# Optimization experiments

Hardware: AMD Instinct MI355X
Metric: run time of the kernel (lower is better)

## Reference

```python
import jax, jax.numpy as jnp
import numpy as np

N_NODES = 100000


def gcn_conv(x, src, dst, deg_inv_sqrt, W, b, n):
    # GCNConv: h = D^{-1/2} (A + I) D^{-1/2} (x W) + b
    h = x @ W                                   # [N, out]
    norm = deg_inv_sqrt[src] * deg_inv_sqrt[dst]  # [E+N]
    msg = h[src] * norm[:, None]                # gather + scale
    out = jax.ops.segment_sum(msg, dst, num_segments=n)  # scatter-add
    return out + b


def setup_inputs() -> dict:
    key = jax.random.key(0)
    k1, k2, k3, k4 = jax.random.split(key, 4)
    N, E, IN, H, C = N_NODES, 1600000, 256, 128, 16
    x = jax.random.normal(k1, (N, IN), dtype=jnp.float32)
    edge_index = jax.random.randint(k2, (2, E), 0, N, dtype=jnp.int64)
    W1 = jax.random.normal(k3, (IN, H), dtype=jnp.float32) * (1.0 / np.sqrt(IN))
    b1 = jnp.zeros((H,), dtype=jnp.float32)
    W2 = jax.random.normal(k4, (H, C), dtype=jnp.float32) * (1.0 / np.sqrt(H))
    b2 = jnp.zeros((C,), dtype=jnp.float32)
    return {"x": x, "edge_index": edge_index, "W1": W1, "b1": b1, "W2": W2, "b2": b2}


def reference(x, edge_index, W1, b1, W2, b2):
    n = x.shape[0]
    loop = jnp.arange(n, dtype=edge_index.dtype)
    src = jnp.concatenate([edge_index[0], loop])  # add self-loops
    dst = jnp.concatenate([edge_index[1], loop])
    deg = jax.ops.segment_sum(jnp.ones_like(src, dtype=x.dtype), dst, num_segments=n)
    deg_inv_sqrt = jax.lax.rsqrt(deg)  # deg >= 1 due to self-loops

    h = gcn_conv(x, src, dst, deg_inv_sqrt, W1, b1, n)
    h = jax.nn.relu(h)
    # dropout is identity in eval mode
    out = gcn_conv(h, src, dst, deg_inv_sqrt, W2, b2, n)
    return jax.nn.log_softmax(out, axis=1)
```

## Files before the change

kernel.cpp:

```cpp
#include <hip/hip_runtime.h>
#include <math.h>

#define IN_DIM 256
#define H_DIM  128
#define C_DIM  16
#define BK_SHIFT 8
#define BK_CAP   6144
#define CHUNK    4096

typedef __attribute__((ext_vector_type(8))) short bf16x8;
typedef __attribute__((ext_vector_type(4))) float f32x4;

__device__ __forceinline__ ushort f2bf(float f) {
    uint u = __float_as_uint(f);
    u += 0x7fffu + ((u >> 16) & 1u);
    return (ushort)(u >> 16);
}
__device__ __forceinline__ float bflo(uint v) { return __uint_as_float(v << 16); }
__device__ __forceinline__ float bfhi(uint v) { return __uint_as_float(v & 0xffff0000u); }
__device__ __forceinline__ uint pk2(float a, float b) {
    return (uint)f2bf(a) | ((uint)f2bf(b) << 16);
}

__global__ void k_zero(int* __restrict__ p, int n) {
    int i = blockIdx.x * blockDim.x + threadIdx.x;
    if (i < n) p[i] = 0;
}

__global__ __launch_bounds__(256) void k_part(const int* __restrict__ esrc, const int* __restrict__ edst, int E,
                                              int* __restrict__ bcnt, int2* __restrict__ part) {
    __shared__ int sh_cnt[512];
    __shared__ int sh_base[512];
    __shared__ int sh_gbase[512];
    __shared__ int sh_scan[256];
    __shared__ int2 sh_rec[CHUNK];
    int t = threadIdx.x;
    int c0 = blockIdx.x * CHUNK;
    int cnt = min(CHUNK, E - c0);
    sh_cnt[t] = 0; sh_cnt[t + 256] = 0;
    __syncthreads();
    int srcv[16], dstv[16], lrank[16];
#pragma unroll
    for (int j = 0; j < 16; j++) {
        int li = j * 256 + t;
        if (li < cnt) {
            srcv[j] = esrc[c0 + li]; dstv[j] = edst[c0 + li];
            lrank[j] = atomicAdd(&sh_cnt[dstv[j] >> BK_SHIFT], 1);
        }
    }
    __syncthreads();
    int pairsum = sh_cnt[2 * t] + sh_cnt[2 * t + 1];
    sh_scan[t] = pairsum;
    __syncthreads();
    for (int off = 1; off < 256; off <<= 1) {
        int x = 0;
        if (t >= off) x = sh_scan[t - off];
        __syncthreads();
        if (t >= off) sh_scan[t] += x;
        __syncthreads();
    }
    int excl = sh_scan[t] - pairsum;
    sh_base[2 * t] = excl;
    sh_base[2 * t + 1] = excl + sh_cnt[2 * t];
    __syncthreads();
    for (int b = t; b < 512; b += 256) {
        int c = sh_cnt[b];
        if (c > 0) sh_gbase[b] = atomicAdd(&bcnt[b], c);
    }
#pragma unroll
    for (int j = 0; j < 16; j++) {
        int li = j * 256 + t;
        if (li < cnt) {
            int b = dstv[j] >> BK_SHIFT;
            sh_rec[sh_base[b] + lrank[j]] = make_int2(srcv[j], dstv[j]);
        }
    }
    __syncthreads();
    for (int idx = t; idx < cnt; idx += 256) {
        int2 r = sh_rec[idx];
        int b = r.y >> BK_SHIFT;
        int pos = sh_gbase[b] + (idx - sh_base[b]);
        if (pos < BK_CAP) part[(size_t)b * BK_CAP + pos] = r;
    }
}

__global__ __launch_bounds__(256) void k_bscan(const int* __restrict__ bcnt, int* __restrict__ bkbase,
                                               int* __restrict__ offsets, int N) {
    __shared__ int sh_scan[256];
    int t = threadIdx.x;
    int a0 = bcnt[2 * t], a1 = bcnt[2 * t + 1];
    int pairsum = a0 + a1;
    sh_scan[t] = pairsum;
    __syncthreads();
    for (int off = 1; off < 256; off <<= 1) {
        int x = 0;
        if (t >= off) x = sh_scan[t - off];
        __syncthreads();
        if (t >= off) sh_scan[t] += x;
        __syncthreads();
    }
    int excl = sh_scan[t] - pairsum;
    bkbase[2 * t] = excl;
    bkbase[2 * t + 1] = excl + a0;
    if (t == 255) offsets[N] = sh_scan[255];
}

__global__ __launch_bounds__(256) void k_bsort(const int* __restrict__ bcnt, const int* __restrict__ bkbase,
                                               const int2* __restrict__ part,
                                               float* __restrict__ dis, int* __restrict__ offsets,
                                               int* __restrict__ csr, int N) {
    __shared__ int hist[256];
    __shared__ int run[256];
    __shared__ int srt[BK_CAP];
    int b = blockIdx.x, t = threadIdx.x;
    hist[t] = 0;
    __syncthreads();
    int cnt = min(bcnt[b], BK_CAP);
    const int2* bp = &part[(size_t)b * BK_CAP];
    for (int idx = t; idx < cnt; idx += 256)
        atomicAdd(&hist[bp[idx].y & 255], 1);
    __syncthreads();
    int v = hist[t];
    run[t] = v;
    __syncthreads();
    for (int off = 1; off < 256; off <<= 1) {
        int x = 0;
        if (t >= off) x = run[t - off];
        __syncthreads();
        if (t >= off) run[t] += x;
        __syncthreads();
    }
    int start = run[t] - v;
    int base = bkbase[b];
    int node = b * 256 + t;
    if (node < N) {
        dis[node] = rsqrtf((float)(v + 1));
        offsets[node] = base + start;
    }
    __syncthreads();
    run[t] = start;
    __syncthreads();
    for (int idx = t; idx < cnt; idx += 256) {
        int2 r = bp[idx];
        int lpos = atomicAdd(&run[r.y & 255], 1);
        srt[lpos] = r.x;
    }
    __syncthreads();
    for (int idx = t; idx < cnt; idx += 256)
        csr[base + idx] = srt[idx];
}

__global__ void k_w1cast(const float* __restrict__ W1, ushort* __restrict__ W1T) {
    int n = blockIdx.x, k = threadIdx.x;
    W1T[n * 256 + k] = f2bf(W1[k * 128 + n]);
}

__global__ __launch_bounds__(256) void k_gemm1(const float* __restrict__ x,
                                               const ushort* __restrict__ W1T,
                                               ushort* __restrict__ h1, int N) {
    __shared__ ushort Al[128 * 64];
    __shared__ ushort Bl[128 * 64];
    int tid = threadIdx.x;
    int lane = tid & 63, wid = tid >> 6;
    int wr = wid >> 1, wc = wid & 1;
    int r0 = blockIdx.x * 128;
    int row16 = lane & 15, kgrp = lane >> 4;

    f32x4 acc[4][4];
#pragma unroll
    for (int i = 0; i < 4; i++)
#pragma unroll
        for (int j = 0; j < 4; j++) acc[i][j] = (f32x4){0.f, 0.f, 0.f, 0.f};

    int srow = tid >> 1, shalf = tid & 1;

    for (int k0 = 0; k0 < 256; k0 += 64) {
        {
            int gr = r0 + srow;
            float4 f[8];
            if (gr < N) {
                const float* xp = &x[(size_t)gr * 256 + k0 + shalf * 32];
#pragma unroll
                for (int j = 0; j < 8; j++) f[j] = *(const float4*)&xp[j * 4];
            } else {
#pragma unroll
                for (int j = 0; j < 8; j++) f[j] = make_float4(0.f, 0.f, 0.f, 0.f);
            }
#pragma unroll
            for (int j = 0; j < 4; j++) {
                uint4 w;
                w.x = pk2(f[2 * j].x, f[2 * j].y);
                w.y = pk2(f[2 * j].z, f[2 * j].w);
                w.z = pk2(f[2 * j + 1].x, f[2 * j + 1].y);
                w.w = pk2(f[2 * j + 1].z, f[2 * j + 1].w);
                int idx = (srow * 64 + shalf * 32 + j * 8) ^ ((srow & 7) << 3);
                *(uint4*)&Al[idx] = w;
            }
        }
        {
            const ushort* wp = &W1T[srow * 256 + k0 + shalf * 32];
#pragma unroll
            for (int j = 0; j < 4; j++) {
                uint4 w = *(const uint4*)&wp[j * 8];
                int idx = (srow * 64 + shalf * 32 + j * 8) ^ ((srow & 7) << 3);
                *(uint4*)&Bl[idx] = w;
            }
        }
        __syncthreads();
#pragma unroll
        for (int kk = 0; kk < 2; kk++) {
            bf16x8 a[4], b[4];
#pragma unroll
            for (int mi = 0; mi < 4; mi++) {
                int r = wr * 64 + mi * 16 + row16;
                a[mi] = *(const bf16x8*)&Al[(r * 64 + kk * 32 + kgrp * 8) ^ ((r & 7) << 3)];
            }
#pragma unroll
            for (int ni = 0; ni < 4; ni++) {
                int c = wc * 64 + ni * 16 + row16;
                b[ni] = *(const bf16x8*)&Bl[(c * 64 + kk * 32 + kgrp * 8) ^ ((c & 7) << 3)];
            }
#pragma unroll
            for (int mi = 0; mi < 4; mi++)
#pragma unroll
                for (int ni = 0; ni < 4; ni++)
                    acc[mi][ni] = __builtin_amdgcn_mfma_f32_16x16x32_bf16(
                        a[mi], b[ni], acc[mi][ni], 0, 0, 0);
        }
        __syncthreads();
    }
#pragma unroll
    for (int mi = 0; mi < 4; mi++) {
        int rbase = r0 + wr * 64 + mi * 16 + kgrp * 4;
#pragma unroll
        for (int ni = 0; ni < 4; ni++) {
            int col = wc * 64 + ni * 16 + row16;
#pragma unroll
            for (int r = 0; r < 4; r++) {
                int gr = rbase + r;
                if (gr < N) h1[(size_t)gr * 128 + col] = f2bf(acc[mi][ni][r]);
            }
        }
    }
}

__global__ __launch_bounds__(256) void k_agg1(const ushort* __restrict__ h1,
                                              const float* __restrict__ dis,
                                              const int* __restrict__ off,
                                              const int* __restrict__ csr,
                                              const float* __restrict__ b1,
                                              const float* __restrict__ W2,
                                              ushort* __restrict__ h2, int N) {
    __shared__ float sh[4][128];
    int wave = threadIdx.x >> 6;
    int lane = threadIdx.x & 63;
    int node = blockIdx.x * 4 + wave;
    if (node >= N) return;

    int grp = lane >> 4, c = lane & 15;
    float w2r[32];
#pragma unroll
    for (int j = 0; j < 32; j++) w2r[j] = W2[(grp * 32 + j) * 16 + c];
    float2 bl = *(const float2*)&b1[lane * 2];

    float dd = dis[node];
    const uint* hp = (const uint*)h1;
    uint a = hp[(size_t)node * 64 + lane];
    float accx = bflo(a) * dd, accy = bfhi(a) * dd;

    int p0 = off[node], p1 = off[node + 1];
    for (int pb = p0; pb < p1; pb += 64) {
        int rem64 = p1 - pb;
        int cnt = rem64 < 64 ? rem64 : 64;
        int s = 0; float w = 0.f;
        if (lane < cnt) { s = csr[pb + lane]; w = dis[s]; }
        int j = 0;
        for (; j + 8 <= cnt; j += 8) {
            uint v[8]; float ww[8];
#pragma unroll
            for (int u = 0; u < 8; u++) {
                int ss = __shfl(s, j + u);
                ww[u] = __shfl(w, j + u);
                v[u] = hp[(size_t)ss * 64 + lane];
            }
#pragma unroll
            for (int u = 0; u < 8; u++) {
                accx += bflo(v[u]) * ww[u];
                accy += bfhi(v[u]) * ww[u];
            }
        }
        int rem = cnt - j;
        if (rem) {
            uint v[8]; float ww[8];
#pragma unroll
            for (int u = 0; u < 8; u++) {
                int ss = __shfl(s, j + u);
                float t = __shfl(w, j + u);
                ww[u] = (u < rem) ? t : 0.f;
                v[u] = (u < rem) ? hp[(size_t)ss * 64 + lane] : 0u;
            }
#pragma unroll
            for (int u = 0; u < 8; u++) {
                accx += bflo(v[u]) * ww[u];
                accy += bfhi(v[u]) * ww[u];
            }
        }
    }
    accx = fmaxf(accx * dd + bl.x, 0.f);
    accy = fmaxf(accy * dd + bl.y, 0.f);
    sh[wave][lane * 2]     = accx;
    sh[wave][lane * 2 + 1] = accy;
    float cs = 0.f;
#pragma unroll
    for (int j = 0; j < 32; j++) cs += sh[wave][grp * 32 + j] * w2r[j];
    cs += __shfl_xor(cs, 16);
    cs += __shfl_xor(cs, 32);
    if (lane < 16) h2[(size_t)node * 16 + lane] = f2bf(cs);
}

__global__ __launch_bounds__(256) void k_final(const ushort* __restrict__ h2,
                                               const float* __restrict__ b2,
                                               const float* __restrict__ dis,
                                               const int* __restrict__ off,
                                               const int* __restrict__ csr,
                                               float* __restrict__ out, int N) {
    int g = threadIdx.x >> 2;
    int q = threadIdx.x & 3;
    int node = blockIdx.x * 64 + g;
    if (node >= N) return;
    float dd = dis[node];
    uint2 v0 = *(const uint2*)&h2[(size_t)node * 16 + q * 4];
    float a0 = bflo(v0.x) * dd, a1 = bfhi(v0.x) * dd;
    float a2 = bflo(v0.y) * dd, a3 = bfhi(v0.y) * dd;
    int p0 = off[node], p1 = off[node + 1];
    for (int pb = p0; pb < p1; pb += 4) {
        int rem4 = p1 - pb;
        int cnt = rem4 < 4 ? rem4 : 4;
        int s = 0; float w = 0.f;
        if (q < cnt) { s = csr[pb + q]; w = dis[s]; }
        uint2 vv[4]; float ww[4];
#pragma unroll
        for (int u = 0; u < 4; u++) {
            int ss = __shfl(s, u, 4);
            float t = __shfl(w, u, 4);
            ww[u] = (u < cnt) ? t : 0.f;
            if (u < cnt) vv[u] = *(const uint2*)&h2[(size_t)ss * 16 + q * 4];
            else         vv[u] = make_uint2(0u, 0u);
        }
#pragma unroll
        for (int u = 0; u < 4; u++) {
            a0 += bflo(vv[u].x) * ww[u]; a1 += bfhi(vv[u].x) * ww[u];
            a2 += bflo(vv[u].y) * ww[u]; a3 += bfhi(vv[u].y) * ww[u];
        }
    }
    a0 = a0 * dd + b2[q * 4 + 0];
    a1 = a1 * dd + b2[q * 4 + 1];
    a2 = a2 * dd + b2[q * 4 + 2];
    a3 = a3 * dd + b2[q * 4 + 3];
    float m = fmaxf(fmaxf(a0, a1), fmaxf(a2, a3));
    m = fmaxf(m, __shfl_xor(m, 1, 4));
    m = fmaxf(m, __shfl_xor(m, 2, 4));
    float s4 = expf(a0 - m) + expf(a1 - m) + expf(a2 - m) + expf(a3 - m);
    s4 += __shfl_xor(s4, 1, 4);
    s4 += __shfl_xor(s4, 2, 4);
    float l = m + logf(s4);
    f32x4 o = {a0 - l, a1 - l, a2 - l, a3 - l};
    *(f32x4*)&out[(size_t)node * 16 + q * 4] = o;
}

extern "C" void kernel_launch(void* const* d_in, const int* in_sizes, int n_in,
                              void* d_out, int out_size, void* d_ws, size_t ws_size,
                              hipStream_t stream) {
    const float* x    = (const float*)d_in[0];
    const int*   eidx = (const int*)d_in[1];
    const float* W1   = (const float*)d_in[2];
    const float* b1   = (const float*)d_in[3];
    const float* W2   = (const float*)d_in[4];
    const float* b2   = (const float*)d_in[5];
    float* out = (float*)d_out;

    int N = in_sizes[0] / IN_DIM;
    int E = in_sizes[1] / 2;
    const int* esrc = eidx;
    const int* edst = eidx + E;

    char* ws = (char*)d_ws;
    size_t wo = 0;
    auto alloc = [&](size_t bytes) -> void* {
        void* p = ws + wo;
        wo = (wo + bytes + 255) & ~(size_t)255;
        return p;
    };
    int NB = (N + 255) >> 8;

    float*  dis     = (float*)alloc((size_t)N * 4);
    int*    offsets = (int*)alloc((size_t)(N + 1) * 4);
    int*    bcnt    = (int*)alloc(512 * 4);
    int*    bkbase  = (int*)alloc(512 * 4);
    int2*   part    = (int2*)alloc((size_t)NB * BK_CAP * 8);
    int*    csr     = (int*)alloc((size_t)E * 4);
    ushort* W1T     = (ushort*)alloc((size_t)IN_DIM * H_DIM * 2);
    ushort* h1      = (ushort*)alloc((size_t)N * H_DIM * 2);
    ushort* h2      = (ushort*)alloc((size_t)N * C_DIM * 2);

    k_zero  <<<2, 256, 0, stream>>>(bcnt, 512);
    k_part  <<<(E + CHUNK - 1) / CHUNK, 256, 0, stream>>>(esrc, edst, E, bcnt, part);
    k_bscan <<<1, 256, 0, stream>>>(bcnt, bkbase, offsets, N);
    k_bsort <<<NB, 256, 0, stream>>>(bcnt, bkbase, part, dis, offsets, csr, N);
    k_w1cast<<<H_DIM, IN_DIM, 0, stream>>>(W1, W1T);

    k_gemm1 <<<(N + 127) / 128, 256, 0, stream>>>(x, W1T, h1, N);
    k_agg1  <<<(N + 3) / 4, 256, 0, stream>>>(h1, dis, offsets, csr, b1, W2, h2, N);
    k_final <<<(N + 63) / 64, 256, 0, stream>>>(h2, b2, dis, offsets, csr, out, N);
}
```

Before: 175.4 us.

## Pack partition records into 32-bit words, merge prep kernels, widen gather unroll

Result: slower. 199.6 us (+13.8%).

```diff
diff --git a/kernel.cpp b/kernel.cpp
--- a/kernel.cpp
+++ b/kernel.cpp
@@ -22,13 +22,16 @@
     return (uint)f2bf(a) | ((uint)f2bf(b) << 16);
 }
 
-__global__ void k_zero(int* __restrict__ p, int n) {
-    int i = blockIdx.x * blockDim.x + threadIdx.x;
-    if (i < n) p[i] = 0;
+__global__ __launch_bounds__(256) void k_prep(int* __restrict__ bcnt,
+                                              const float* __restrict__ W1, ushort* __restrict__ W1T) {
+    int b = blockIdx.x, t = threadIdx.x;
+    if (b < 2) { bcnt[b * 256 + t] = 0; return; }
+    int n = b - 2;
+    W1T[n * 256 + t] = f2bf(W1[t * 128 + n]);
 }
 
 __global__ __launch_bounds__(256) void k_part(const int* __restrict__ esrc, const int* __restrict__ edst, int E,
-                                              int* __restrict__ bcnt, int2* __restrict__ part) {
+                                              int* __restrict__ bcnt, int* __restrict__ part) {
     __shared__ int sh_cnt[512];
     __shared__ int sh_base[512];
     __shared__ int sh_gbase[512];
@@ -80,7 +83,8 @@
         int2 r = sh_rec[idx];
         int b = r.y >> BK_SHIFT;
         int pos = sh_gbase[b] + (idx - sh_base[b]);
-        if (pos < BK_CAP) part[(size_t)b * BK_CAP + pos] = r;
+        if (pos < BK_CAP)
+            part[(size_t)b * BK_CAP + pos] = r.x | ((r.y & 255) << 20);
     }
 }
 
@@ -106,7 +110,7 @@
 }
 
 __global__ __launch_bounds__(256) void k_bsort(const int* __restrict__ bcnt, const int* __restrict__ bkbase,
-                                               const int2* __restrict__ part,
+                                               const int* __restrict__ part,
                                                float* __restrict__ dis, int* __restrict__ offsets,
                                                int* __restrict__ csr, int N) {
     __shared__ int hist[256];
@@ -116,9 +120,9 @@
     hist[t] = 0;
     __syncthreads();
     int cnt = min(bcnt[b], BK_CAP);
-    const int2* bp = &part[(size_t)b * BK_CAP];
+    const int* bp = &part[(size_t)b * BK_CAP];
     for (int idx = t; idx < cnt; idx += 256)
-        atomicAdd(&hist[bp[idx].y & 255], 1);
+        atomicAdd(&hist[bp[idx] >> 20], 1);
     __syncthreads();
     int v = hist[t];
     run[t] = v;
@@ -141,18 +145,13 @@
     run[t] = start;
     __syncthreads();
     for (int idx = t; idx < cnt; idx += 256) {
-        int2 r = bp[idx];
-        int lpos = atomicAdd(&run[r.y & 255], 1);
-        srt[lpos] = r.x;
+        int r = bp[idx];
+        int lpos = atomicAdd(&run[r >> 20], 1);
+        srt[lpos] = r & 0xFFFFF;
     }
     __syncthreads();
     for (int idx = t; idx < cnt; idx += 256)
         csr[base + idx] = srt[idx];
-}
-
-__global__ void k_w1cast(const float* __restrict__ W1, ushort* __restrict__ W1T) {
-    int n = blockIdx.x, k = threadIdx.x;
-    W1T[n * 256 + k] = f2bf(W1[k * 128 + n]);
 }
 
 __global__ __launch_bounds__(256) void k_gemm1(const float* __restrict__ x,
@@ -270,37 +269,22 @@
 
     int p0 = off[node], p1 = off[node + 1];
     for (int pb = p0; pb < p1; pb += 64) {
-        int rem64 = p1 - pb;
-        int cnt = rem64 < 64 ? rem64 : 64;
+        int cnt = min(64, p1 - pb);
         int s = 0; float w = 0.f;
         if (lane < cnt) { s = csr[pb + lane]; w = dis[s]; }
-        int j = 0;
-        for (; j + 8 <= cnt; j += 8) {
-            uint v[8]; float ww[8];
-#pragma unroll
-            for (int u = 0; u < 8; u++) {
-                int ss = __shfl(s, j + u);
-                ww[u] = __shfl(w, j + u);
-                v[u] = hp[(size_t)ss * 64 + lane];
-            }
-#pragma unroll
-            for (int u = 0; u < 8; u++) {
-                accx += bflo(v[u]) * ww[u];
-                accy += bfhi(v[u]) * ww[u];
-            }
-        }
-        int rem = cnt - j;
-        if (rem) {
-            uint v[8]; float ww[8];
-#pragma unroll
-            for (int u = 0; u < 8; u++) {
-                int ss = __shfl(s, j + u);
-                float t = __shfl(w, j + u);
-                ww[u] = (u < rem) ? t : 0.f;
-                v[u] = (u < rem) ? hp[(size_t)ss * 64 + lane] : 0u;
-            }
-#pragma unroll
-            for (int u = 0; u < 8; u++) {
+        for (int j = 0; j < cnt; j += 16) {
+            uint v[16]; float ww[16];
+#pragma unroll
+            for (int u = 0; u < 16; u++) {
+                int idx = j + u;
+                int ss = __shfl(s, idx);
+                float t = __shfl(w, idx);
+                bool pr = idx < cnt;
+                ww[u] = pr ? t : 0.f;
+                v[u] = pr ? hp[(size_t)ss * 64 + lane] : 0u;
+            }
+#pragma unroll
+            for (int u = 0; u < 16; u++) {
                 accx += bflo(v[u]) * ww[u];
                 accy += bfhi(v[u]) * ww[u];
             }
@@ -397,17 +381,16 @@
     int*    offsets = (int*)alloc((size_t)(N + 1) * 4);
     int*    bcnt    = (int*)alloc(512 * 4);
     int*    bkbase  = (int*)alloc(512 * 4);
-    int2*   part    = (int2*)alloc((size_t)NB * BK_CAP * 8);
+    int*    part    = (int*)alloc((size_t)NB * BK_CAP * 4);
     int*    csr     = (int*)alloc((size_t)E * 4);
     ushort* W1T     = (ushort*)alloc((size_t)IN_DIM * H_DIM * 2);
     ushort* h1      = (ushort*)alloc((size_t)N * H_DIM * 2);
     ushort* h2      = (ushort*)alloc((size_t)N * C_DIM * 2);
 
-    k_zero  <<<2, 256, 0, stream>>>(bcnt, 512);
+    k_prep  <<<130, 256, 0, stream>>>(bcnt, W1, W1T);
     k_part  <<<(E + CHUNK - 1) / CHUNK, 256, 0, stream>>>(esrc, edst, E, bcnt, part);
     k_bscan <<<1, 256, 0, stream>>>(bcnt, bkbase, offsets, N);
     k_bsort <<<NB, 256, 0, stream>>>(bcnt, bkbase, part, dis, offsets, csr, N);
-    k_w1cast<<<H_DIM, IN_DIM, 0, stream>>>(W1, W1T);
 
     k_gemm1 <<<(N + 127) / 128, 256, 0, stream>>>(x, W1T, h1, N);
     k_agg1  <<<(N + 3) / 4, 256, 0, stream>>>(h1, dis, offsets, csr, b1, W2, h2, N);
```
